# Performance work log

Hardware: AMD Instinct MI355X
Metric: run time of the kernel (lower is better)

## Reference

```python
import jax, jax.numpy as jnp
import numpy as np

EMB = 128
WINDOW = 200
D_K = 32
D_V = 32
NUM_H = 8
COS_EPS = 1e-6


def setup_inputs() -> dict:
    key = jax.random.key(0)
    ks = jax.random.split(key, 12)
    b, n_t, n_c = 1024, 50, WINDOW
    s = 1.0 / np.sqrt(EMB)
    inp = {
        "queries": jax.random.normal(ks[0], (b, n_t, EMB), jnp.float32),
        "keys": jax.random.normal(ks[1], (b, n_c, EMB), jnp.float32),
        "values": jax.random.normal(ks[2], (b, n_c, EMB), jnp.float32),
        # nn.Linear weights: (out_features, in_features)
        "At_w": jax.random.uniform(ks[3], (NUM_H * D_K, EMB), jnp.float32, -s, s),
        "At_b": jax.random.uniform(ks[4], (NUM_H * D_K,), jnp.float32, -s, s),
        "Ac_w": jax.random.uniform(ks[5], (NUM_H * D_K, EMB), jnp.float32, -s, s),
        "Ac_b": jax.random.uniform(ks[6], (NUM_H * D_K,), jnp.float32, -s, s),
        "Bc_w": jax.random.uniform(ks[7], (NUM_H * D_V, EMB), jnp.float32, -s, s),
        "Bc_b": jax.random.uniform(ks[8], (NUM_H * D_V,), jnp.float32, -s, s),
        "pos_bias": jax.random.uniform(ks[9], (WINDOW,), jnp.float32, -0.5 / WINDOW, 0.5 / WINDOW),
        "R_w": jax.random.uniform(ks[10], (EMB, NUM_H * D_V), jnp.float32, -1.0 / np.sqrt(NUM_H * D_V), 1.0 / np.sqrt(NUM_H * D_V)),
        "R_b": jax.random.uniform(ks[11], (EMB,), jnp.float32, -1.0 / np.sqrt(NUM_H * D_V), 1.0 / np.sqrt(NUM_H * D_V)),
    }
    return inp


def reference(queries, keys, values, At_w, At_b, Ac_w, Ac_b, Bc_w, Bc_b, pos_bias, R_w, R_b):
    b, n_t, _ = queries.shape
    n_c = keys.shape[1]
    # projections -> (b, h, n, d)
    q = (queries @ At_w.T + At_b).reshape(b, n_t, NUM_H, D_K).transpose(0, 2, 1, 3)
    k = (keys @ Ac_w.T + Ac_b).reshape(b, n_c, NUM_H, D_K).transpose(0, 2, 1, 3)
    v = (values @ Bc_w.T + Bc_b).reshape(b, n_c, NUM_H, D_V).transpose(0, 2, 1, 3)
    # cosine similarity attention scores (b, h, n_t, n_c)
    dots = jnp.einsum("bhtd,bhcd->bhtc", q, k)
    qn = jnp.sqrt(jnp.sum(q * q, axis=-1))  # (b,h,n_t)
    kn = jnp.sqrt(jnp.sum(k * k, axis=-1))  # (b,h,n_c)
    denom = jnp.maximum(qn[..., :, None] * kn[..., None, :], COS_EPS)
    att = dots / denom + pos_bias  # pos_bias broadcasts over last dim (n_c == window)
    att = jax.nn.softmax(att, axis=-1)
    out = jnp.einsum("bhtc,bhcd->bhtd", att, v)  # (b,h,n_t,d_v)
    out = out.transpose(0, 2, 1, 3).reshape(b, n_t, NUM_H * D_V)
    out = out @ R_w.T + R_b  # (b, n_t, emb)
    return out, att
```

## Files before the change

kernel.cpp:

```cpp
#include <hip/hip_runtime.h>


#define NT 50
#define NC 200
#define EMB 128
#define DH 32
#define NH 8
#define THREADS 512
#define LOG2E 1.44269504088896340736f

#define WS_PROJ_LO 98304u
#define WS_R_HI    196608u
#define WS_R_LO    229376u
#define WS_PSW     262144u
#define WS_PLANES_B 720896u

typedef __attribute__((ext_vector_type(4))) float f4acc;
typedef __attribute__((ext_vector_type(8))) short bh8;

__device__ __forceinline__ f4acc mfma_bf16(bh8 a, bh8 b, f4acc c) {
    return __builtin_amdgcn_mfma_f32_16x16x32_bf16(a, b, c, 0, 0, 0);
}

__device__ __forceinline__ unsigned short bf16rne(float x) {
    unsigned int u = __float_as_uint(x);
    u += 0x7FFFu + ((u >> 16) & 1u);
    return (unsigned short)(u >> 16);
}

__device__ __forceinline__ bh8 cvt8(const float* __restrict__ p) {
    float4 x0 = *reinterpret_cast<const float4*>(p);
    float4 x1 = *reinterpret_cast<const float4*>(p + 4);
    float xs[8] = {x0.x, x0.y, x0.z, x0.w, x1.x, x1.y, x1.z, x1.w};
    union { unsigned int w[4]; bh8 v; } H;
    #pragma unroll
    for (int i = 0; i < 4; ++i)
        asm("v_cvt_pk_bf16_f32 %0, %1, %2"
            : "=v"(H.w[i]) : "v"(xs[2 * i]), "v"(xs[2 * i + 1]));
    return H.v;
}

__device__ __forceinline__ void split8(const float* __restrict__ p, bh8& hi, bh8& lo) {
    float4 x0 = *reinterpret_cast<const float4*>(p);
    float4 x1 = *reinterpret_cast<const float4*>(p + 4);
    float xs[8] = {x0.x, x0.y, x0.z, x0.w, x1.x, x1.y, x1.z, x1.w};
    union { unsigned int w[4]; bh8 v; } H, L;
    #pragma unroll
    for (int i = 0; i < 4; ++i) {
        const float a = xs[2 * i], b = xs[2 * i + 1];
        unsigned int hw, lw;
        asm("v_cvt_pk_bf16_f32 %0, %1, %2" : "=v"(hw) : "v"(a), "v"(b));
        const float ha = __uint_as_float(hw << 16);
        const float hb = __uint_as_float(hw & 0xFFFF0000u);
        const float la = a - ha, lb = b - hb;
        asm("v_cvt_pk_bf16_f32 %0, %1, %2" : "=v"(lw) : "v"(la), "v"(lb));
        H.w[i] = hw; L.w[i] = lw;
    }
    hi = H.v; lo = L.v;
}

__global__ __launch_bounds__(512) void wprep(
    const float* __restrict__ At_w, const float* __restrict__ Ac_w,
    const float* __restrict__ Bc_w, const float* __restrict__ R_w,
    unsigned short* __restrict__ ws)
{
    const int u = blockIdx.x * 512 + threadIdx.x;
    bh8 h8, l8;
    if (u < 12288) {
        const int p = u >> 12, rem = u & 4095;
        const int col = rem >> 4, e0 = (rem & 15) << 3;
        const float* W = (p == 0) ? At_w : (p == 1) ? Ac_w : Bc_w;
        split8(W + (size_t)col * 128 + e0, h8, l8);
        const size_t o = ((size_t)p * 256 + col) * 128 + e0;
        *reinterpret_cast<bh8*>(ws + o) = h8;
        *reinterpret_cast<bh8*>(ws + WS_PROJ_LO + o) = l8;
    } else if (u < 16384) {
        const int u2 = u - 12288;
        const int e = u2 >> 5, k0 = (u2 & 31) << 3;
        split8(R_w + (size_t)e * 256 + k0, h8, l8);
        const size_t o = (size_t)e * 256 + k0;
        *reinterpret_cast<bh8*>(ws + WS_R_HI + o) = h8;
        *reinterpret_cast<bh8*>(ws + WS_R_LO + o) = l8;
    } else {
        const int u2 = u - 16384;
        const int lane = u2 & 63;
        const int ks = (u2 >> 6) & 3;
        const int colgrp = (u2 >> 8) & 1;
        const int head = (u2 >> 9) & 7;
        const int ty = u2 >> 12;
        const float* W = (ty == 0) ? At_w : (ty == 1) ? Ac_w : Bc_w;
        const int col = head * 32 + colgrp * 16 + (lane & 15);
        const int g = lane >> 4;
        *reinterpret_cast<bh8*>(ws + WS_PSW + (size_t)u2 * 8) =
            cvt8(W + (size_t)col * 128 + ks * 32 + g * 8);
    }
}

__device__ __forceinline__ void projn_wfrag(
    const unsigned short* __restrict__ wsp, int ty, int head, int lane,
    bh8* bf0, bh8* bf1)
{
    const unsigned short* base = wsp + WS_PSW + ((size_t)(ty * 8 + head) << 12)
                               + (size_t)lane * 8;
    #pragma unroll
    for (int ks = 0; ks < 4; ++ks) {
        bf0[ks] = *reinterpret_cast<const bh8*>(base + (ks << 9));
        bf1[ks] = *reinterpret_cast<const bh8*>(base + 2048 + (ks << 9));
    }
}

__device__ __forceinline__ void tinfo(int r, int& ty, int& mt, int& nrows) {
    ty = (r < 4) ? 0 : (r < 17) ? 1 : 2;
    mt = r - ((ty == 0) ? 0 : (ty == 1) ? 4 : 17);
    nrows = (ty == 0) ? NT : NC;
}

__global__ __launch_bounds__(512, 6) void projn(
    const float* __restrict__ gq, const float* __restrict__ gk,
    const float* __restrict__ gv,
    const float* __restrict__ At_b, const float* __restrict__ Ac_b,
    const float* __restrict__ Bc_b,
    const unsigned short* __restrict__ wsp,
    unsigned short* __restrict__ qh, unsigned short* __restrict__ kh,
    unsigned short* __restrict__ vh)
{
    __shared__ __align__(16) float sX[2][16][132];
    __shared__ __align__(16) unsigned short sO[16 * 264];

    const int blk = blockIdx.x;
    const int b = blk / 3, third = blk - b * 3;
    const int t = threadIdx.x;
    const int lane = t & 63, head = t >> 6, l15 = lane & 15, g = lane >> 4;
    const int c0i = head * 32 + l15, c1i = c0i + 16;
    const int srow = t >> 5, scol = (t & 31) * 4;
    const int fr = lane >> 2, fc = lane & 3;

    const float* Xb[3] = {gq + (size_t)b * NT * EMB,
                          gk + (size_t)b * NC * EMB,
                          gv + (size_t)b * NC * EMB};
    unsigned short* Ob[3] = {qh + (size_t)b * (NT * 256),
                             kh + (size_t)b * (NC * 256),
                             vh + (size_t)b * (NC * 256)};
    const float* Bb[3] = {At_b, Ac_b, Bc_b};

    const int r0 = third * 10;
    int ty, mt, nrows;
    tinfo(r0, ty, mt, nrows);

    {
        int row = mt * 16 + srow; if (row > nrows - 1) row = nrows - 1;
        *reinterpret_cast<float4*>(&sX[0][srow][scol]) =
            *reinterpret_cast<const float4*>(Xb[ty] + (size_t)row * EMB + scol);
    }
    bh8 bf0[4], bf1[4];
    projn_wfrag(wsp, ty, head, lane, bf0, bf1);
    float bias0 = Bb[ty][c0i], bias1 = Bb[ty][c1i];
    __syncthreads();

    for (int i = 0; i < 10; ++i) {
        const int cur = i & 1;
        const int cty = ty, cmt = mt, cnrows = nrows;

        float4 xreg;
        const bool have_next = (i + 1 < 10);
        int nty = ty, nmt = mt, nnrows = nrows;
        if (have_next) {
            tinfo(r0 + i + 1, nty, nmt, nnrows);
            int row = nmt * 16 + srow; if (row > nnrows - 1) row = nnrows - 1;
            xreg = *reinterpret_cast<const float4*>(
                Xb[nty] + (size_t)row * EMB + scol);
        }

        f4acc a0 = {bias0, bias0, bias0, bias0};
        f4acc a1 = {bias1, bias1, bias1, bias1};
        #pragma unroll
        for (int ks = 0; ks < 4; ++ks) {
            const bh8 xv = cvt8(&sX[cur][l15][ks * 32 + (g << 3)]);
            a0 = mfma_bf16(xv, bf0[ks], a0);
            a1 = mfma_bf16(xv, bf1[ks], a1);
        }
        if (cty < 2) {
            float s[4];
            #pragma unroll
            for (int rr = 0; rr < 4; ++rr) s[rr] = a0[rr] * a0[rr] + a1[rr] * a1[rr];
            #pragma unroll
            for (int rr = 0; rr < 4; ++rr) {
                s[rr] += __shfl_xor(s[rr], 1);
                s[rr] += __shfl_xor(s[rr], 2);
                s[rr] += __shfl_xor(s[rr], 4);
                s[rr] += __shfl_xor(s[rr], 8);
            }
            #pragma unroll
            for (int rr = 0; rr < 4; ++rr) {
                const float rs = rsqrtf(fmaxf(s[rr], 1e-12f));
                a0[rr] *= rs; a1[rr] *= rs;
            }
        }
        #pragma unroll
        for (int rr = 0; rr < 4; ++rr) {
            const int row = (g << 2) + rr;
            sO[row * 264 + c0i] = bf16rne(a0[rr]);
            sO[row * 264 + c1i] = bf16rne(a1[rr]);
        }
        asm volatile("" ::: "memory");
        {
            const int grow = cmt * 16 + fr;
            if (grow < cnrows)
                *reinterpret_cast<bh8*>(
                    Ob[cty] + (size_t)grow * 256 + head * 32 + fc * 8) =
                    *reinterpret_cast<const bh8*>(&sO[fr * 264 + head * 32 + fc * 8]);
        }
        if (have_next) {
            *reinterpret_cast<float4*>(&sX[cur ^ 1][srow][scol]) = xreg;
            if (nty != cty) {
                projn_wfrag(wsp, nty, head, lane, bf0, bf1);
                bias0 = Bb[nty][c0i]; bias1 = Bb[nty][c1i];
            }
            ty = nty; mt = nmt; nrows = nnrows;
        }
        __syncthreads();
    }
}

__global__ __launch_bounds__(512, 6) void attn2(
    const unsigned short* __restrict__ qh, const unsigned short* __restrict__ kh,
    const unsigned short* __restrict__ vh, const float* __restrict__ pos_bias,
    float* __restrict__ att, float* __restrict__ cat, int nbat)
{
    const int t = threadIdx.x;
    const int p = blockIdx.x;
    const int chunk = (nbat * NH) >> 3;
    const int lj = (p & 7) * chunk + (p >> 3);
    const int b = lj >> 3, h = lj & 7;
    const int lane = t & 63, wave = t >> 6, l15 = lane & 15, g = lane >> 4;

    __shared__ __align__(16) unsigned char smem[39872];
    unsigned short* sVT = reinterpret_cast<unsigned short*>(smem);
    unsigned short* sK  = reinterpret_cast<unsigned short*>(smem + 14848);
    unsigned short* sQ  = reinterpret_cast<unsigned short*>(smem + 30848);
    unsigned short* sP  = reinterpret_cast<unsigned short*>(smem + 14848);
    float* spb = reinterpret_cast<float*>(smem + 38048);
    float* sSm = reinterpret_cast<float*>(smem + 39360);

    if (t < 448) {
        unsigned int* v32 = reinterpret_cast<unsigned int*>(sVT);
        const int col = t / 14, i = t - col * 14;
        v32[col * 116 + 100 + i] = 0u;
    }
    if (t < NC) spb[t] = pos_bias[t] * LOG2E;
    if (t < 200) {
        const int row = t >> 2, q = t & 3;
        *reinterpret_cast<bh8*>(sQ + row * 40 + q * 8) =
            *reinterpret_cast<const bh8*>(qh + (size_t)b * (NT * 256) + row * 256 + h * 32 + q * 8);
    }
    for (int u = t; u < 800; u += THREADS) {
        const int row = u >> 2, q = u & 3;
        *reinterpret_cast<bh8*>(sK + row * 40 + q * 8) =
            *reinterpret_cast<const bh8*>(kh + (size_t)b * (NC * 256) + row * 256 + h * 32 + q * 8);
    }
    for (int u = t; u < 800; u += THREADS) {
        const int row = u >> 2, q = u & 3;
        const bh8 vv = *reinterpret_cast<const bh8*>(
            vh + (size_t)b * (NC * 256) + row * 256 + h * 32 + q * 8);
        #pragma unroll
        for (int e = 0; e < 8; ++e)
            sVT[(q * 8 + e) * 232 + row] = (unsigned short)vv[e];
    }
    __syncthreads();

    const int mt = wave & 3, hf = wave >> 2;
    const int m0 = mt << 4;
    const int row64 = m0 + (g << 2);
    int arow = m0 + l15; if (arow > NT - 1) arow = NT - 1;
    const bh8 aq = *reinterpret_cast<const bh8*>(sQ + arow * 40 + (g << 3));

    f4acc acc[7];
    #pragma unroll
    for (int i = 0; i < 7; ++i) {
        const int nt = hf * 7 + i;
        if (nt < 13) {
            const int col = (nt << 4) + l15;
            const int bc = (col < NC) ? col : (NC - 1);
            const bh8 bk = *reinterpret_cast<const bh8*>(sK + bc * 40 + (g << 3));
            f4acc c = {0.f, 0.f, 0.f, 0.f};
            c = mfma_bf16(aq, bk, c);
            const float pbl = spb[bc];
            #pragma unroll
            for (int r = 0; r < 4; ++r)
                acc[i][r] = (col < NC) ? fmaf(c[r], LOG2E, pbl) : -1e30f;
        }
    }
    __syncthreads();

    {
        unsigned int* p32 = reinterpret_cast<unsigned int*>(sP);
        for (int tt = t; tt < 700; tt += THREADS) {
            const int row = tt / 14, i = tt - row * 14;
            p32[row * 116 + 100 + i] = 0u;
        }
    }
    {
        float sl[4] = {0.f, 0.f, 0.f, 0.f};
        #pragma unroll
        for (int i = 0; i < 7; ++i) {
            if (hf * 7 + i < 13) {
                #pragma unroll
                for (int r = 0; r < 4; ++r) {
                    const float e = __builtin_exp2f(acc[i][r]);
                    acc[i][r] = e;
                    sl[r] += e;
                }
            }
        }
        #pragma unroll
        for (int r = 0; r < 4; ++r) {
            sl[r] += __shfl_xor(sl[r], 1);
            sl[r] += __shfl_xor(sl[r], 2);
            sl[r] += __shfl_xor(sl[r], 4);
            sl[r] += __shfl_xor(sl[r], 8);
        }
        if (l15 == 0) {
            #pragma unroll
            for (int r = 0; r < 4; ++r) sSm[hf * 64 + row64 + r] = sl[r];
        }
    }
    __syncthreads();

    {
        float inv[4];
        #pragma unroll
        for (int r = 0; r < 4; ++r)
            inv[r] = 1.0f / (sSm[row64 + r] + sSm[64 + row64 + r]);
        float* attb = att + (size_t)(b * NH + h) * NT * NC;
        #pragma unroll
        for (int i = 0; i < 7; ++i) {
            const int nt = hf * 7 + i;
            if (nt < 13) {
                const int col = (nt << 4) + l15;
                if (col < NC) {
                    #pragma unroll
                    for (int r = 0; r < 4; ++r) {
                        const int row = row64 + r;
                        if (row < NT) {
                            const float v = acc[i][r] * inv[r];
                            attb[row * NC + col] = v;
                            sP[row * 232 + col] = bf16rne(v);
                        }
                    }
                }
            }
        }
    }
    __syncthreads();

    {
        const int pnt = wave >> 2;
        const unsigned short* pA = sP + arow * 232;
        const unsigned short* pB = sVT + (size_t)((pnt << 4) + l15) * 232;
        f4acc o = {0.f, 0.f, 0.f, 0.f};
        #pragma unroll
        for (int ks = 0; ks < 7; ++ks) {
            const bh8 a = *reinterpret_cast<const bh8*>(pA + ks * 32 + (g << 3));
            const bh8 v = *reinterpret_cast<const bh8*>(pB + ks * 32 + (g << 3));
            o = mfma_bf16(a, v, o);
        }
        float* wsb = cat + (size_t)b * (NT * NH * DH) + h * DH;
        #pragma unroll
        for (int r = 0; r < 4; ++r) {
            const int row = row64 + r;
            if (row < NT) wsb[(size_t)row * (NH * DH) + (pnt << 4) + l15] = o[r];
        }
    }
}

template <int WSP>
__global__ __launch_bounds__(THREADS, 4) void attn_mfma(
    const float* __restrict__ gq, const float* __restrict__ gk,
    const float* __restrict__ gv,
    const float* __restrict__ At_w, const float* __restrict__ At_b,
    const float* __restrict__ Ac_w, const float* __restrict__ Ac_b,
    const float* __restrict__ Bc_w, const float* __restrict__ Bc_b,
    const float* __restrict__ pos_bias,
    const float* __restrict__ R_w, const float* __restrict__ R_b,
    float* __restrict__ out, float* __restrict__ att,
    float* __restrict__ cat, const unsigned short* __restrict__ wsp,
    int nbat)
{
    const int t = threadIdx.x;
    const int p = blockIdx.x;
    const int chunk = (nbat * NH) >> 3;
    const int lj = (p & 7) * chunk + (p >> 3);
    const int b = lj >> 3;
    const int h = lj & 7;
    const int lane = t & 63, wave = t >> 6;
    const int l15 = lane & 15, g = lane >> 4;

    __shared__ __align__(16) unsigned char smem[39872];
    unsigned short* sVT = reinterpret_cast<unsigned short*>(smem);
    unsigned short* sK  = reinterpret_cast<unsigned short*>(smem + 14848);
    unsigned short* sQ  = reinterpret_cast<unsigned short*>(smem + 30848);
    unsigned short* sP  = reinterpret_cast<unsigned short*>(smem + 14848);
    float* spb = reinterpret_cast<float*>(smem + 38048);
    float* sSm = reinterpret_cast<float*>(smem + 39360);

    if (t < 448) {
        unsigned int* v32 = reinterpret_cast<unsigned int*>(sVT);
        const int col = t / 14, i = t - col * 14;
        v32[col * 116 + 100 + i] = 0u;
    }
    if (t < NC) spb[t] = pos_bias[t] * LOG2E;

    {
        const int s0 = (wave * 60) >> 3;
        const int s1 = ((wave + 1) * 60) >> 3;
        int cp = -1, cn = -1;
        bh8 wh[4], wl[4];
        float bias = 0.f;
        for (int id = s0; id < s1; ++id) {
            int pidx, nt, mt2;
            if (id < 8)       { pidx = 0; nt = id >> 2; mt2 = id & 3; }
            else if (id < 34) { int jj = id - 8;  pidx = 1; nt = jj / 13; mt2 = jj - nt * 13; }
            else              { int jj = id - 34; pidx = 2; nt = jj / 13; mt2 = jj - nt * 13; }
            const int col = (nt << 4) + l15;
            if (pidx != cp || nt != cn) {
                cp = pidx; cn = nt;
                const int gcol = h * DH + col;
                if (WSP) {
                    const unsigned short* whp =
                        wsp + ((size_t)pidx * 256 + gcol) * 128 + (g << 3);
                    const unsigned short* wlp = whp + WS_PROJ_LO;
                    #pragma unroll
                    for (int ks = 0; ks < 4; ++ks) {
                        wh[ks] = *reinterpret_cast<const bh8*>(whp + ks * 32);
                        wl[ks] = *reinterpret_cast<const bh8*>(wlp + ks * 32);
                    }
                } else {
                    const float* Wm = (pidx == 0) ? At_w : (pidx == 1) ? Ac_w : Bc_w;
                    const float* bp = Wm + (size_t)gcol * EMB + (g << 3);
                    #pragma unroll
                    for (int ks = 0; ks < 4; ++ks) split8(bp + ks * 32, wh[ks], wl[ks]);
                }
                const float* Wb = (pidx == 0) ? At_b : (pidx == 1) ? Ac_b : Bc_b;
                bias = Wb[gcol];
            }
            const int nrows = (pidx == 0) ? NT : NC;
            const float* Xbp = (pidx == 0) ? gq : (pidx == 1) ? gk : gv;
            int ar = mt2 * 16 + l15; if (ar > nrows - 1) ar = nrows - 1;
            const float* ap = Xbp + (size_t)b * nrows * EMB + (size_t)ar * EMB + (g << 3);
            f4acc acc2 = {bias, bias, bias, bias};
            #pragma unroll
            for (int ks = 0; ks < 4; ++ks) {
                bh8 xh, xl;
                split8(ap + ks * 32, xh, xl);
                acc2 = mfma_bf16(xh, wh[ks], acc2);
                acc2 = mfma_bf16(xl, wh[ks], acc2);
                acc2 = mfma_bf16(xh, wl[ks], acc2);
            }
            #pragma unroll
            for (int r = 0; r < 4; ++r) {
                const int row = mt2 * 16 + (g << 2) + r;
                if (row < nrows) {
                    const unsigned short hv = bf16rne(acc2[r]);
                    if (pidx == 0)      sQ[row * 40 + col] = hv;
                    else if (pidx == 1) sK[row * 40 + col] = hv;
                    else                sVT[col * 232 + row] = hv;
                }
            }
        }
    }
    __syncthreads();

    if (t < 250) {
        unsigned short* rowp = (t < 200) ? (sK + t * 40) : (sQ + (t - 200) * 40);
        unsigned int* w32 = reinterpret_cast<unsigned int*>(rowp);
        unsigned int w[16];
        #pragma unroll
        for (int i = 0; i < 16; ++i) w[i] = w32[i];
        float s = 0.f;
        #pragma unroll
        for (int i = 0; i < 16; ++i) {
            const float a = __uint_as_float(w[i] << 16);
            const float c = __uint_as_float(w[i] & 0xFFFF0000u);
            s += a * a + c * c;
        }
        const float rs = rsqrtf(fmaxf(s, 1e-12f));
        #pragma unroll
        for (int i = 0; i < 16; ++i) {
            const float a = __uint_as_float(w[i] << 16) * rs;
            const float c = __uint_as_float(w[i] & 0xFFFF0000u) * rs;
            unsigned int pw;
            asm("v_cvt_pk_bf16_f32 %0, %1, %2" : "=v"(pw) : "v"(a), "v"(c));
            w32[i] = pw;
        }
    }
    __syncthreads();

    const int mt = wave & 3, hf = wave >> 2;
    const int m0 = mt << 4;
    const int row64 = m0 + (g << 2);
    int arow = m0 + l15; if (arow > NT - 1) arow = NT - 1;
    const bh8 aq = *reinterpret_cast<const bh8*>(sQ + arow * 40 + (g << 3));

    f4acc acc[7];
    #pragma unroll
    for (int i = 0; i < 7; ++i) {
        const int nt = hf * 7 + i;
        if (nt < 13) {
            const int col = (nt << 4) + l15;
            const int bc = (col < NC) ? col : (NC - 1);
            const bh8 bk = *reinterpret_cast<const bh8*>(sK + bc * 40 + (g << 3));
            f4acc c = {0.f, 0.f, 0.f, 0.f};
            c = mfma_bf16(aq, bk, c);
            const float pbl = spb[bc];
            #pragma unroll
            for (int r = 0; r < 4; ++r)
                acc[i][r] = (col < NC) ? fmaf(c[r], LOG2E, pbl) : -1e30f;
        }
    }
    __syncthreads();

    {
        unsigned int* p32 = reinterpret_cast<unsigned int*>(sP);
        for (int tt = t; tt < 700; tt += THREADS) {
            const int row = tt / 14, i = tt - row * 14;
            p32[row * 116 + 100 + i] = 0u;
        }
    }
    {
        float sl[4] = {0.f, 0.f, 0.f, 0.f};
        #pragma unroll
        for (int i = 0; i < 7; ++i) {
            if (hf * 7 + i < 13) {
                #pragma unroll
                for (int r = 0; r < 4; ++r) {
                    const float e = __builtin_exp2f(acc[i][r]);
                    acc[i][r] = e;
                    sl[r] += e;
                }
            }
        }
        #pragma unroll
        for (int r = 0; r < 4; ++r) {
            sl[r] += __shfl_xor(sl[r], 1);
            sl[r] += __shfl_xor(sl[r], 2);
            sl[r] += __shfl_xor(sl[r], 4);
            sl[r] += __shfl_xor(sl[r], 8);
        }
        if (l15 == 0) {
            #pragma unroll
            for (int r = 0; r < 4; ++r) sSm[hf * 64 + row64 + r] = sl[r];
        }
    }
    __syncthreads();

    {
        float inv[4];
        #pragma unroll
        for (int r = 0; r < 4; ++r)
            inv[r] = 1.0f / (sSm[row64 + r] + sSm[64 + row64 + r]);
        float* attb = att + (size_t)(b * NH + h) * NT * NC;
        #pragma unroll
        for (int i = 0; i < 7; ++i) {
            const int nt = hf * 7 + i;
            if (nt < 13) {
                const int col = (nt << 4) + l15;
                if (col < NC) {
                    #pragma unroll
                    for (int r = 0; r < 4; ++r) {
                        const int row = row64 + r;
                        if (row < NT) {
                            const float v = acc[i][r] * inv[r];
                            attb[row * NC + col] = v;
                            sP[row * 232 + col] = bf16rne(v);
                        }
                    }
                }
            }
        }
    }
    __syncthreads();

    {
        const int pnt = wave >> 2;
        const unsigned short* pA = sP + arow * 232;
        const unsigned short* pB = sVT + (size_t)((pnt << 4) + l15) * 232;
        f4acc o = {0.f, 0.f, 0.f, 0.f};
        #pragma unroll
        for (int ks = 0; ks < 7; ++ks) {
            const bh8 a = *reinterpret_cast<const bh8*>(pA + ks * 32 + (g << 3));
            const bh8 v = *reinterpret_cast<const bh8*>(pB + ks * 32 + (g << 3));
            o = mfma_bf16(a, v, o);
        }
        if (WSP) {
            float* wsb = cat + (size_t)b * (NT * NH * DH) + h * DH;
            #pragma unroll
            for (int r = 0; r < 4; ++r) {
                const int row = row64 + r;
                if (row < NT) wsb[(size_t)row * (NH * DH) + (pnt << 4) + l15] = o[r];
            }
        } else {
            __syncthreads();
            float* sOH = reinterpret_cast<float*>(smem);
            #pragma unroll
            for (int r = 0; r < 4; ++r) {
                const int row = row64 + r;
                if (row < NT) sOH[row * DH + (pnt << 4) + l15] = o[r];
            }
            __syncthreads();
            for (int oo = t; oo < NT * EMB; oo += THREADS) {
                const int r = oo >> 7, e = oo & 127;
                float s = (h == 0) ? R_b[e] : 0.f;
                const float* rw = R_w + (size_t)e * (NH * DH) + h * DH;
                const float* oh = sOH + r * DH;
                #pragma unroll
                for (int c = 0; c < DH; ++c) s += oh[c] * rw[c];
                atomicAdd(&out[((size_t)b * NT + r) * EMB + e], s);
            }
        }
    }
}

__global__ __launch_bounds__(256, 4) void rproj4(
    const float* __restrict__ cat, const unsigned short* __restrict__ rhi,
    const float* __restrict__ R_b, float* __restrict__ out)
{
    const int t = threadIdx.x;
    const int lane = t & 63, wave = t >> 6;
    const int l15 = lane & 15, g = lane >> 4;
    const int m0 = blockIdx.x * 64 + wave * 16;
    const float* ap = cat + (size_t)(m0 + l15) * 256 + (g << 3);
    const unsigned short* rlo = rhi + (WS_R_LO - WS_R_HI);

    f4acc acc[8];
    #pragma unroll
    for (int nt = 0; nt < 8; ++nt) {
        const float rb = R_b[nt * 16 + l15];
        acc[nt][0] = rb; acc[nt][1] = rb; acc[nt][2] = rb; acc[nt][3] = rb;
    }
    #pragma unroll
    for (int ks = 0; ks < 8; ++ks) {
        bh8 ah, al;
        split8(ap + ks * 32, ah, al);
        #pragma unroll
        for (int nt = 0; nt < 8; ++nt) {
            const size_t o = (size_t)(nt * 16 + l15) * 256 + ks * 32 + (g << 3);
            const bh8 bh_ = *reinterpret_cast<const bh8*>(rhi + o);
            const bh8 bl_ = *reinterpret_cast<const bh8*>(rlo + o);
            acc[nt] = mfma_bf16(ah, bh_, acc[nt]);
            acc[nt] = mfma_bf16(al, bh_, acc[nt]);
            acc[nt] = mfma_bf16(ah, bl_, acc[nt]);
        }
    }
    const int row = m0 + (g << 2);
    #pragma unroll
    for (int nt = 0; nt < 8; ++nt) {
        #pragma unroll
        for (int r = 0; r < 4; ++r)
            out[(size_t)(row + r) * EMB + nt * 16 + l15] = acc[nt][r];
    }
}

extern "C" void kernel_launch(void* const* d_in, const int* in_sizes, int n_in,
                              void* d_out, int out_size, void* d_ws, size_t ws_size,
                              hipStream_t stream)
{
    const float* gq   = (const float*)d_in[0];
    const float* gk   = (const float*)d_in[1];
    const float* gv   = (const float*)d_in[2];
    const float* At_w = (const float*)d_in[3];
    const float* At_b = (const float*)d_in[4];
    const float* Ac_w = (const float*)d_in[5];
    const float* Ac_b = (const float*)d_in[6];
    const float* Bc_w = (const float*)d_in[7];
    const float* Bc_b = (const float*)d_in[8];
    const float* pb   = (const float*)d_in[9];
    const float* R_w  = (const float*)d_in[10];
    const float* R_b  = (const float*)d_in[11];

    const int nbat = in_sizes[0] / (NT * EMB);
    float* out = (float*)d_out;
    float* att = out + (size_t)nbat * NT * EMB;

    const size_t qB   = (size_t)nbat * NT * 256 * 2;
    const size_t kB   = (size_t)nbat * NC * 256 * 2;
    const size_t catB = (size_t)nbat * NT * NH * DH * sizeof(float);
    const size_t need3 = WS_PLANES_B + qB + 2 * kB + catB;
    const size_t need2 = WS_PLANES_B + catB;
    const int nwg = nbat * NH;

    if (ws_size >= need3) {
        unsigned short* wsp = (unsigned short*)d_ws;
        unsigned short* qh = (unsigned short*)((char*)d_ws + WS_PLANES_B);
        unsigned short* kh = (unsigned short*)((char*)d_ws + WS_PLANES_B + qB);
        unsigned short* vh = (unsigned short*)((char*)d_ws + WS_PLANES_B + qB + kB);
        float* cat = (float*)((char*)d_ws + WS_PLANES_B + qB + 2 * kB);
        wprep<<<56, 512, 0, stream>>>(At_w, Ac_w, Bc_w, R_w, wsp);
        projn<<<nbat * 3, 512, 0, stream>>>(gq, gk, gv, At_b, Ac_b, Bc_b,
                                            wsp, qh, kh, vh);
        attn2<<<nwg, THREADS, 0, stream>>>(qh, kh, vh, pb, att, cat, nbat);
        rproj4<<<(nbat * NT) / 64, 256, 0, stream>>>(cat, wsp + WS_R_HI, R_b, out);
    } else if (ws_size >= need2) {
        unsigned short* wsp = (unsigned short*)d_ws;
        float* cat = (float*)((char*)d_ws + WS_PLANES_B);
        wprep<<<56, 512, 0, stream>>>(At_w, Ac_w, Bc_w, R_w, wsp);
        attn_mfma<1><<<nwg, THREADS, 0, stream>>>(
            gq, gk, gv, At_w, At_b, Ac_w, Ac_b, Bc_w, Bc_b, pb, R_w, R_b,
            out, att, cat, wsp, nbat);
        rproj4<<<(nbat * NT) / 64, 256, 0, stream>>>(cat, wsp + WS_R_HI, R_b, out);
    } else {
        hipMemsetAsync(d_out, 0, (size_t)nbat * NT * EMB * sizeof(float), stream);
        attn_mfma<0><<<nwg, THREADS, 0, stream>>>(
            gq, gk, gv, At_w, At_b, Ac_w, Ac_b, Bc_w, Bc_b, pb, R_w, R_b,
            out, att, nullptr, nullptr, nbat);
    }
}
```

Measured before the change: 355.0 us.

## Deepen projection prefetch to two tiles and raise occupancy bounds

The projection kernel now prefetches input tiles two iterations ahead in registers instead of one, giving global loads more time to arrive before they are staged into shared memory. Indexed pointer arrays are replaced with ternary macros so the compiler does not spill them to scratch memory. Both projn and attn2 raise their launch-bounds minimum blocks hint from 6 to 8, which caps register use per thread. The tighter register cap, together with the extra in-flight prefetch registers, could cause spilling.

```diff
diff --git a/kernel.cpp b/kernel.cpp
--- a/kernel.cpp
+++ b/kernel.cpp
@@ -115,7 +115,7 @@
     nrows = (ty == 0) ? NT : NC;
 }
 
-__global__ __launch_bounds__(512, 6) void projn(
+__global__ __launch_bounds__(512, 8) void projn(
     const float* __restrict__ gq, const float* __restrict__ gk,
     const float* __restrict__ gv,
     const float* __restrict__ At_b, const float* __restrict__ Ac_b,
@@ -135,13 +135,13 @@
     const int srow = t >> 5, scol = (t & 31) * 4;
     const int fr = lane >> 2, fc = lane & 3;
 
-    const float* Xb[3] = {gq + (size_t)b * NT * EMB,
-                          gk + (size_t)b * NC * EMB,
-                          gv + (size_t)b * NC * EMB};
-    unsigned short* Ob[3] = {qh + (size_t)b * (NT * 256),
-                             kh + (size_t)b * (NC * 256),
-                             vh + (size_t)b * (NC * 256)};
-    const float* Bb[3] = {At_b, Ac_b, Bc_b};
+    #define XBASE(TY) ((TY) == 0 ? gq + (size_t)b * NT * EMB \
+                      : (TY) == 1 ? gk + (size_t)b * NC * EMB \
+                                  : gv + (size_t)b * NC * EMB)
+    #define OBASE(TY) ((TY) == 0 ? qh + (size_t)b * (NT * 256) \
+                      : (TY) == 1 ? kh + (size_t)b * (NC * 256) \
+                                  : vh + (size_t)b * (NC * 256))
+    #define BBASE(TY) ((TY) == 0 ? At_b : (TY) == 1 ? Ac_b : Bc_b)
 
     const int r0 = third * 10;
     int ty, mt, nrows;
@@ -150,25 +150,33 @@
     {
         int row = mt * 16 + srow; if (row > nrows - 1) row = nrows - 1;
         *reinterpret_cast<float4*>(&sX[0][srow][scol]) =
-            *reinterpret_cast<const float4*>(Xb[ty] + (size_t)row * EMB + scol);
+            *reinterpret_cast<const float4*>(XBASE(ty) + (size_t)row * EMB + scol);
     }
     bh8 bf0[4], bf1[4];
     projn_wfrag(wsp, ty, head, lane, bf0, bf1);
-    float bias0 = Bb[ty][c0i], bias1 = Bb[ty][c1i];
+    float bias0 = BBASE(ty)[c0i], bias1 = BBASE(ty)[c1i];
+
+    int tyA, mtA, nrA;
+    tinfo(r0 + 1, tyA, mtA, nrA);
+    float4 xregA;
+    {
+        int row = mtA * 16 + srow; if (row > nrA - 1) row = nrA - 1;
+        xregA = *reinterpret_cast<const float4*>(
+            XBASE(tyA) + (size_t)row * EMB + scol);
+    }
     __syncthreads();
 
     for (int i = 0; i < 10; ++i) {
         const int cur = i & 1;
         const int cty = ty, cmt = mt, cnrows = nrows;
 
-        float4 xreg;
-        const bool have_next = (i + 1 < 10);
-        int nty = ty, nmt = mt, nnrows = nrows;
-        if (have_next) {
-            tinfo(r0 + i + 1, nty, nmt, nnrows);
-            int row = nmt * 16 + srow; if (row > nnrows - 1) row = nnrows - 1;
-            xreg = *reinterpret_cast<const float4*>(
-                Xb[nty] + (size_t)row * EMB + scol);
+        float4 xregB;
+        int tyB = tyA, mtB = mtA, nrB = nrA;
+        if (i + 2 < 10) {
+            tinfo(r0 + i + 2, tyB, mtB, nrB);
+            int row = mtB * 16 + srow; if (row > nrB - 1) row = nrB - 1;
+            xregB = *reinterpret_cast<const float4*>(
+                XBASE(tyB) + (size_t)row * EMB + scol);
         }
 
         f4acc a0 = {bias0, bias0, bias0, bias0};
@@ -207,22 +215,27 @@
             const int grow = cmt * 16 + fr;
             if (grow < cnrows)
                 *reinterpret_cast<bh8*>(
-                    Ob[cty] + (size_t)grow * 256 + head * 32 + fc * 8) =
+                    OBASE(cty) + (size_t)grow * 256 + head * 32 + fc * 8) =
                     *reinterpret_cast<const bh8*>(&sO[fr * 264 + head * 32 + fc * 8]);
         }
-        if (have_next) {
-            *reinterpret_cast<float4*>(&sX[cur ^ 1][srow][scol]) = xreg;
-            if (nty != cty) {
-                projn_wfrag(wsp, nty, head, lane, bf0, bf1);
-                bias0 = Bb[nty][c0i]; bias1 = Bb[nty][c1i];
-            }
-            ty = nty; mt = nmt; nrows = nnrows;
+        if (i + 1 < 10) {
+            *reinterpret_cast<float4*>(&sX[cur ^ 1][srow][scol]) = xregA;
+            if (tyA != cty) {
+                projn_wfrag(wsp, tyA, head, lane, bf0, bf1);
+                bias0 = BBASE(tyA)[c0i]; bias1 = BBASE(tyA)[c1i];
+            }
+            ty = tyA; mt = mtA; nrows = nrA;
+            tyA = tyB; mtA = mtB; nrA = nrB;
+            xregA = xregB;
         }
         __syncthreads();
     }
-}
-
-__global__ __launch_bounds__(512, 6) void attn2(
+    #undef XBASE
+    #undef OBASE
+    #undef BBASE
+}
+
+__global__ __launch_bounds__(512, 8) void attn2(
     const unsigned short* __restrict__ qh, const unsigned short* __restrict__ kh,
     const unsigned short* __restrict__ vh, const float* __restrict__ pos_bias,
     float* __restrict__ att, float* __restrict__ cat, int nbat)
```

New measurement: 475.7 us. 34.0% more time.
